# Performance work log

Hardware: AMD Instinct MI355X
Metric: run time of the kernel (lower is better)

Reference implementation:

```python
import jax, jax.numpy as jnp
import numpy as np

B, N, C, R = 8, 1024, 256, 16


def setup_inputs() -> dict:
    key = jax.random.key(0)
    kq, kk, kwq, kwk, kbq, kbk, kr = jax.random.split(key, 7)
    init = 0.02
    return {
        "query_states": jax.random.normal(kq, (B, N, C), dtype=jnp.float32),
        "key_states": jax.random.normal(kk, (B, N, C), dtype=jnp.float32),
        "W_q": jax.random.normal(kwq, (C, C), dtype=jnp.float32) * init,
        "b_q": jax.random.normal(kbq, (C,), dtype=jnp.float32) * init,
        "W_k": jax.random.normal(kwk, (C, C), dtype=jnp.float32) * init,
        "b_k": jax.random.normal(kbk, (C,), dtype=jnp.float32) * init,
        "R_map": jax.random.normal(kr, (N, N, R), dtype=jnp.float32),
    }


def reference(query_states, key_states, W_q, b_q, W_k, b_k, R_map):
    input_dtype = query_states.dtype
    c = query_states.shape[-1]
    # Q/K linear projections (torch Linear: x @ W.T + b)
    qh = query_states @ W_q.T + b_q  # (B, N, C)
    kh = key_states @ W_k.T + b_k    # (B, N, C)
    # batched QK^T score in fp32 (original casts to float32 before bmm)
    scores = jnp.einsum(
        "bic,bjc->bij", qh.astype(jnp.float32), kh.astype(jnp.float32)
    ) / jnp.sqrt(jnp.asarray(c, jnp.float32))  # (B, N, N)
    # elementwise relation-mask multiply: broadcast over relation axis
    rel_mask = jnp.transpose(R_map, (2, 0, 1))  # (R, N, N)
    relation = scores[:, None, :, :] * rel_mask[None]  # (B, R, N, N)
    return relation.astype(input_dtype)
```

## Files before the change

kernel.cpp:

```cpp
#include <hip/hip_runtime.h>
#include <hip/hip_bf16.h>


typedef float  floatx4 __attribute__((ext_vector_type(4)));
typedef short  shortx8 __attribute__((ext_vector_type(8)));

__device__ __forceinline__ short f2bf(float f) {
    unsigned int u = __builtin_bit_cast(unsigned int, f);
    u += 0x7fffu + ((u >> 16) & 1u);
    return (short)(u >> 16);
}

__global__ __launch_bounds__(64) void proj_kernel(
    const float* __restrict__ Xq, const float* __restrict__ Wq, const float* __restrict__ bq,
    const float* __restrict__ Xk, const float* __restrict__ Wk, const float* __restrict__ bk,
    short* __restrict__ qh, short* __restrict__ kh)
{
    const float* X; const float* W; const float* bias; short* outp;
    if (blockIdx.z == 0) { X = Xq; W = Wq; bias = bq; outp = qh; }
    else                 { X = Xk; W = Wk; bias = bk; outp = kh; }

    const int lane  = threadIdx.x;
    const int row16 = lane & 15;
    const int quad  = lane >> 4;
    const int m0 = blockIdx.x * 16;
    const int c0 = blockIdx.y * 64;

    const float* xr = X + (size_t)(m0 + row16) * 256 + quad * 8;
    const float* wr = W + (size_t)(c0 + row16) * 256 + quad * 8;

    floatx4 acc[4];
#pragma unroll
    for (int nt = 0; nt < 4; nt++) acc[nt] = floatx4{0.f, 0.f, 0.f, 0.f};

#pragma unroll
    for (int k = 0; k < 256; k += 32) {
        float4 a0 = *(const float4*)(xr + k);
        float4 a1 = *(const float4*)(xr + k + 4);
        shortx8 af = { f2bf(a0.x), f2bf(a0.y), f2bf(a0.z), f2bf(a0.w),
                       f2bf(a1.x), f2bf(a1.y), f2bf(a1.z), f2bf(a1.w) };
#pragma unroll
        for (int nt = 0; nt < 4; nt++) {
            const float* w0 = wr + (size_t)nt * 16 * 256 + k;
            float4 b0 = *(const float4*)(w0);
            float4 b1 = *(const float4*)(w0 + 4);
            shortx8 bf = { f2bf(b0.x), f2bf(b0.y), f2bf(b0.z), f2bf(b0.w),
                           f2bf(b1.x), f2bf(b1.y), f2bf(b1.z), f2bf(b1.w) };
            acc[nt] = __builtin_amdgcn_mfma_f32_16x16x32_bf16(af, bf, acc[nt], 0, 0, 0);
        }
    }

#pragma unroll
    for (int nt = 0; nt < 4; nt++) {
        const int c = c0 + nt * 16 + row16;
        const float bv = bias[c];
#pragma unroll
        for (int r = 0; r < 4; r++) {
            const int m = m0 + quad * 4 + r;
            outp[(size_t)m * 256 + c] = f2bf(acc[nt][r] + bv);
        }
    }
}

__global__ __launch_bounds__(256) void score_mul_kernel(
    const short* __restrict__ qh, const short* __restrict__ kh,
    const float* __restrict__ Rm, float* __restrict__ out)
{
    const int itile = blockIdx.x;
    const int b     = blockIdx.y;
    const int i0    = itile * 16;

    const int tid   = threadIdx.x;
    const int w     = tid >> 6;
    const int lane  = tid & 63;
    const int row16 = lane & 15;
    const int quad  = lane >> 4;

    __shared__ float s_lds[16 * 1024];

    const short* qbase = qh + ((size_t)(b * 1024 + i0 + row16)) * 256 + quad * 8;
    shortx8 a[8];
#pragma unroll
    for (int ks = 0; ks < 8; ks++) a[ks] = *(const shortx8*)(qbase + ks * 32);

    const short* kb = kh + ((size_t)(b * 1024 + w * 256 + row16)) * 256 + quad * 8;
    const float inv = 0.0625f;

#pragma unroll 2
    for (int jt = 0; jt < 16; jt++) {
        floatx4 acc = {0.f, 0.f, 0.f, 0.f};
        const short* kr = kb + (size_t)jt * 16 * 256;
#pragma unroll
        for (int ks = 0; ks < 8; ks++) {
            shortx8 bfr = *(const shortx8*)(kr + ks * 32);
            acc = __builtin_amdgcn_mfma_f32_16x16x32_bf16(a[ks], bfr, acc, 0, 0, 0);
        }
#pragma unroll
        for (int r = 0; r < 4; r++)
            s_lds[(quad * 4 + r) * 1024 + w * 256 + jt * 16 + row16] = acc[r] * inv;
    }
    __syncthreads();

    const int jc = w * 256 + lane * 4;
    const size_t NN = (size_t)1024 * 1024;
    float* ob = out + (size_t)(b * 16) * NN + jc;

    for (int il = 0; il < 16; il++) {
        const int i = i0 + il;
        floatx4 s4 = *(const floatx4*)&s_lds[il * 1024 + jc];
        const float* rp = Rm + ((size_t)i * 1024 + jc) * 16;

        floatx4 q[4][4];
#pragma unroll
        for (int jo = 0; jo < 4; jo++)
#pragma unroll
            for (int rg = 0; rg < 4; rg++)
                q[jo][rg] = *(const floatx4*)(rp + jo * 16 + rg * 4);

        float* op = ob + (size_t)i * 1024;
#pragma unroll
        for (int r = 0; r < 16; r++) {
            const int rg = r >> 2, rs = r & 3;
            floatx4 v = { q[0][rg][rs] * s4[0], q[1][rg][rs] * s4[1],
                          q[2][rg][rs] * s4[2], q[3][rg][rs] * s4[3] };
            __builtin_nontemporal_store(v, (floatx4*)(op + (size_t)r * NN));
        }
    }
}

extern "C" void kernel_launch(void* const* d_in, const int* in_sizes, int n_in,
                              void* d_out, int out_size, void* d_ws, size_t ws_size,
                              hipStream_t stream) {
    const float* q   = (const float*)d_in[0];
    const float* k   = (const float*)d_in[1];
    const float* Wq  = (const float*)d_in[2];
    const float* bq  = (const float*)d_in[3];
    const float* Wk  = (const float*)d_in[4];
    const float* bk  = (const float*)d_in[5];
    const float* Rm  = (const float*)d_in[6];
    float* out = (float*)d_out;

    short* qh = (short*)d_ws;
    short* kh = (short*)d_ws + (size_t)8192 * 256;

    dim3 pgrid(512, 4, 2);
    proj_kernel<<<pgrid, 64, 0, stream>>>(q, Wq, bq, k, Wk, bk, qh, kh);

    dim3 sgrid(64, 8);
    score_mul_kernel<<<sgrid, 256, 0, stream>>>(qh, kh, Rm, out);
}
```

Baseline: 668.1 us.

## Split score kernel over column halves to halve LDS and raise occupancy

Adds a third grid dimension that splits each 16-row tile's j range into two halves. This halves the LDS score buffer to 32KB, adds a launch-bounds occupancy hint, and doubles the block count. The multiply-store phase now has each thread cover 8 rows instead of 16, and R_map is loaded in smaller per-group chunks to cut register pressure. The aim is more waves in flight to hide memory latency on the streaming output writes, at the cost of computing the Q fragments twice.

New measurement: 700.4 us. 1.05x slower.

```diff
diff --git a/kernel.cpp b/kernel.cpp
--- a/kernel.cpp
+++ b/kernel.cpp
@@ -62,12 +62,13 @@
     }
 }
 
-__global__ __launch_bounds__(256) void score_mul_kernel(
+__global__ __launch_bounds__(256, 4) void score_mul_kernel(
     const short* __restrict__ qh, const short* __restrict__ kh,
     const float* __restrict__ Rm, float* __restrict__ out)
 {
     const int itile = blockIdx.x;
     const int b     = blockIdx.y;
+    const int h     = blockIdx.z;
     const int i0    = itile * 16;
 
     const int tid   = threadIdx.x;
@@ -76,18 +77,18 @@
     const int row16 = lane & 15;
     const int quad  = lane >> 4;
 
-    __shared__ float s_lds[16 * 1024];
+    __shared__ float s_lds[16 * 512];
 
     const short* qbase = qh + ((size_t)(b * 1024 + i0 + row16)) * 256 + quad * 8;
     shortx8 a[8];
 #pragma unroll
     for (int ks = 0; ks < 8; ks++) a[ks] = *(const shortx8*)(qbase + ks * 32);
 
-    const short* kb = kh + ((size_t)(b * 1024 + w * 256 + row16)) * 256 + quad * 8;
+    const short* kb = kh + ((size_t)(b * 1024 + h * 512 + w * 128 + row16)) * 256 + quad * 8;
     const float inv = 0.0625f;
 
 #pragma unroll 2
-    for (int jt = 0; jt < 16; jt++) {
+    for (int jt = 0; jt < 8; jt++) {
         floatx4 acc = {0.f, 0.f, 0.f, 0.f};
         const short* kr = kb + (size_t)jt * 16 * 256;
 #pragma unroll
@@ -97,33 +98,35 @@
         }
 #pragma unroll
         for (int r = 0; r < 4; r++)
-            s_lds[(quad * 4 + r) * 1024 + w * 256 + jt * 16 + row16] = acc[r] * inv;
+            s_lds[(quad * 4 + r) * 512 + w * 128 + jt * 16 + row16] = acc[r] * inv;
     }
     __syncthreads();
 
-    const int jc = w * 256 + lane * 4;
+    const int ih = tid >> 7;
+    const int jl = (tid & 127) * 4;
+    const int j  = h * 512 + jl;
     const size_t NN = (size_t)1024 * 1024;
-    float* ob = out + (size_t)(b * 16) * NN + jc;
+    float* ob = out + (size_t)(b * 16) * NN + j;
 
-    for (int il = 0; il < 16; il++) {
-        const int i = i0 + il;
-        floatx4 s4 = *(const floatx4*)&s_lds[il * 1024 + jc];
-        const float* rp = Rm + ((size_t)i * 1024 + jc) * 16;
+    for (int il = 0; il < 8; il++) {
+        const int ilocal = ih * 8 + il;
+        const int i = i0 + ilocal;
+        floatx4 s4 = *(const floatx4*)&s_lds[ilocal * 512 + jl];
+        const float* rp = Rm + ((size_t)i * 1024 + j) * 16;
+        float* op = ob + (size_t)i * 1024;
 
-        floatx4 q[4][4];
 #pragma unroll
-        for (int jo = 0; jo < 4; jo++)
+        for (int rg = 0; rg < 4; rg++) {
+            floatx4 q0 = *(const floatx4*)(rp + 0  + rg * 4);
+            floatx4 q1 = *(const floatx4*)(rp + 16 + rg * 4);
+            floatx4 q2 = *(const floatx4*)(rp + 32 + rg * 4);
+            floatx4 q3 = *(const floatx4*)(rp + 48 + rg * 4);
 #pragma unroll
-            for (int rg = 0; rg < 4; rg++)
-                q[jo][rg] = *(const floatx4*)(rp + jo * 16 + rg * 4);
-
-        float* op = ob + (size_t)i * 1024;
-#pragma unroll
-        for (int r = 0; r < 16; r++) {
-            const int rg = r >> 2, rs = r & 3;
-            floatx4 v = { q[0][rg][rs] * s4[0], q[1][rg][rs] * s4[1],
-                          q[2][rg][rs] * s4[2], q[3][rg][rs] * s4[3] };
-            __builtin_nontemporal_store(v, (floatx4*)(op + (size_t)r * NN));
+            for (int rs = 0; rs < 4; rs++) {
+                floatx4 v = { q0[rs] * s4[0], q1[rs] * s4[1],
+                              q2[rs] * s4[2], q3[rs] * s4[3] };
+                __builtin_nontemporal_store(v, (floatx4*)(op + (size_t)(rg * 4 + rs) * NN));
+            }
         }
     }
 }
@@ -146,6 +149,6 @@
     dim3 pgrid(512, 4, 2);
     proj_kernel<<<pgrid, 64, 0, stream>>>(q, Wq, bq, k, Wk, bk, qh, kh);
 
-    dim3 sgrid(64, 8);
+    dim3 sgrid(64, 8, 2);
     score_mul_kernel<<<sgrid, 256, 0, stream>>>(qh, kh, Rm, out);
 }
```
